# Kernel optimization log

Hardware: AMD Instinct MI355X
Metric: run time of the kernel (lower is better)

Reference implementation:

```python
import jax, jax.numpy as jnp
import numpy as np

N_NODES = 50000
HIDDEN = 64
N_EDGES = 1200000


def setup_inputs() -> dict:
    key = jax.random.key(0)
    ks = jax.random.split(key, 12)
    x = jax.random.normal(ks[0], (N_NODES, HIDDEN), dtype=jnp.float32)
    edge_index = jax.random.randint(ks[1], (2, N_EDGES), 0, N_NODES, dtype=jnp.int64)
    s = 1.0 / np.sqrt(HIDDEN)
    # RGCN layer (single relation): relation weight, root weight, bias
    W_rel1 = jax.random.normal(ks[2], (HIDDEN, HIDDEN), dtype=jnp.float32) * s
    W_root1 = jax.random.normal(ks[3], (HIDDEN, HIDDEN), dtype=jnp.float32) * s
    b1 = jnp.zeros((HIDDEN,), dtype=jnp.float32)
    # Three GraphConv layers: self weight, neighbor weight, bias each
    W_self2 = jax.random.normal(ks[4], (HIDDEN, HIDDEN), dtype=jnp.float32) * s
    W_nbr2 = jax.random.normal(ks[5], (HIDDEN, HIDDEN), dtype=jnp.float32) * s
    b2 = jnp.zeros((HIDDEN,), dtype=jnp.float32)
    W_self3 = jax.random.normal(ks[6], (HIDDEN, HIDDEN), dtype=jnp.float32) * s
    W_nbr3 = jax.random.normal(ks[7], (HIDDEN, HIDDEN), dtype=jnp.float32) * s
    b3 = jnp.zeros((HIDDEN,), dtype=jnp.float32)
    W_self4 = jax.random.normal(ks[8], (HIDDEN, HIDDEN), dtype=jnp.float32) * s
    W_nbr4 = jax.random.normal(ks[9], (HIDDEN, HIDDEN), dtype=jnp.float32) * s
    b4 = jnp.zeros((HIDDEN,), dtype=jnp.float32)
    return {
        "x": x, "edge_index": edge_index,
        "W_rel1": W_rel1, "W_root1": W_root1, "b1": b1,
        "W_self2": W_self2, "W_nbr2": W_nbr2, "b2": b2,
        "W_self3": W_self3, "W_nbr3": W_nbr3, "b3": b3,
        "W_self4": W_self4, "W_nbr4": W_nbr4, "b4": b4,
    }


def _rgcn(x, W_rel, W_root, b, src, dst, n_nodes):
    # single-relation RGCN: root transform + mean-aggregated relation transform
    msg = x[src] @ W_rel                                   # [E, H]
    agg = jax.ops.segment_sum(msg, dst, num_segments=n_nodes)
    cnt = jax.ops.segment_sum(jnp.ones((src.shape[0],), x.dtype), dst, num_segments=n_nodes)
    agg = agg / jnp.maximum(cnt, 1.0)[:, None]
    return x @ W_root + agg + b


def _graphconv(x, W_self, W_nbr, b, src, dst, n_nodes):
    # GraphConv: self transform + sum-aggregated neighbor transform
    agg = jax.ops.segment_sum(x[src], dst, num_segments=n_nodes)  # [N, H]
    return x @ W_self + agg @ W_nbr + b


def reference(x, edge_index, W_rel1, W_root1, b1, W_self2, W_nbr2, b2,
              W_self3, W_nbr3, b3, W_self4, W_nbr4, b4):
    n = x.shape[0]
    src, dst = edge_index[0], edge_index[1]
    h = jax.nn.relu(_rgcn(x, W_rel1, W_root1, b1, src, dst, n))
    h = jax.nn.relu(_graphconv(h, W_self2, W_nbr2, b2, src, dst, n))
    x_1 = h
    h = jax.nn.relu(_graphconv(h, W_self3, W_nbr3, b3, src, dst, n))
    h = jax.nn.relu(_graphconv(h, W_self4, W_nbr4, b4, src, dst, n))
    x_2 = h
    return (x_1, x_2)
```

## Files before the change

kernel.cpp:

```cpp
#include <hip/hip_runtime.h>
#include <hip/hip_fp16.h>

#define N_NODES 50000
#define HIDDEN  64
#define N_EDGES 1200000

#define BSHIFT 7
#define BUKSZ  128
#define NBUK   391
#define GBIN   256
#define PAD2   6144
#define FWAVES 12500
#define FBLK   (FWAVES / 4)
#define NPW    4

typedef unsigned short ushort_t;
typedef _Float16 hf2 __attribute__((ext_vector_type(2)));

__device__ __forceinline__ float bcastf(float v, int k) {
    return __int_as_float(__builtin_amdgcn_readlane(__float_as_int(v), k));
}
__device__ __forceinline__ hf2 u2h(unsigned u) { union { unsigned u; hf2 h; } x; x.u = u; return x.h; }
__device__ __forceinline__ unsigned h2u(hf2 h) { union { hf2 h; unsigned u; } x; x.h = h; return x.u; }
__device__ __forceinline__ unsigned pkh(float a, float b) {
    __half2 h = __float22half2_rn(make_float2(a, b));
    union { __half2 h; unsigned u; } x; x.h = h; return x.u;
}
__device__ __forceinline__ ushort_t f2h(float a) {
    __half h = __float2half_rn(a);
    union { __half h; ushort_t u; } x; x.h = h; return x.u;
}
__device__ __forceinline__ void bfly(float4& a) {
    a.x += __shfl_xor(a.x, 16); a.y += __shfl_xor(a.y, 16);
    a.z += __shfl_xor(a.z, 16); a.w += __shfl_xor(a.w, 16);
    a.x += __shfl_xor(a.x, 32); a.y += __shfl_xor(a.y, 32);
    a.z += __shfl_xor(a.z, 32); a.w += __shfl_xor(a.w, 32);
}

__global__ __launch_bounds__(512) void init_kernel(int* __restrict__ cursor,
                                                   const float* __restrict__ Wn2, const float* __restrict__ Ws2,
                                                   const float* __restrict__ Wn3, const float* __restrict__ Ws3,
                                                   const float* __restrict__ Wn4, const float* __restrict__ Ws4,
                                                   uint4* __restrict__ pw) {
    int b = blockIdx.x, tid = threadIdx.x;
    if (b == 0) {
        if (tid < NBUK) cursor[tid] = tid * PAD2;
    } else {
        int layer = b - 1;
        const float* Wn = (layer == 0) ? Wn2 : (layer == 1) ? Wn3 : Wn4;
        const float* Ws = (layer == 0) ? Ws2 : (layer == 1) ? Ws3 : Ws4;
        int kp = tid >> 4, q = tid & 15;
        {
            const float4 a = *(const float4*)(Wn + (2 * kp) * 64 + 4 * q);
            const float4 c = *(const float4*)(Wn + (2 * kp + 1) * 64 + 4 * q);
            pw[layer * 1024 + tid] = make_uint4(pkh(a.x, c.x), pkh(a.y, c.y), pkh(a.z, c.z), pkh(a.w, c.w));
        }
        {
            const float4 a = *(const float4*)(Ws + (2 * kp) * 64 + 4 * q);
            const float4 c = *(const float4*)(Ws + (2 * kp + 1) * 64 + 4 * q);
            pw[layer * 1024 + 512 + tid] = make_uint4(pkh(a.x, c.x), pkh(a.y, c.y), pkh(a.z, c.z), pkh(a.w, c.w));
        }
    }
}

__global__ __launch_bounds__(256) void scatter_fused_kernel(const int* __restrict__ ei,
                                                            int* __restrict__ cursor,
                                                            int* __restrict__ tmp, int E) {
    __shared__ int h[NBUK];
    __shared__ int cur[NBUK];
    int tid = threadIdx.x;
    for (int b = tid; b < NBUK; b += 256) h[b] = 0;
    __syncthreads();
    for (int e = blockIdx.x * 256 + tid; e < E; e += GBIN * 256)
        atomicAdd(&h[ei[E + e] >> BSHIFT], 1);
    __syncthreads();
    for (int b = tid; b < NBUK; b += 256) cur[b] = atomicAdd(&cursor[b], h[b]);
    __syncthreads();
    for (int e = blockIdx.x * 256 + tid; e < E; e += GBIN * 256) {
        int src = ei[e];
        int dst = ei[E + e];
        int p = atomicAdd(&cur[dst >> BSHIFT], 1);
        tmp[p] = src | ((dst & (BUKSZ - 1)) << 16);
    }
}

__global__ __launch_bounds__(512) void bucketize_kernel(const int* __restrict__ tmp,
                                                        const int* __restrict__ cursor,
                                                        int2* __restrict__ row_info,
                                                        ushort_t* __restrict__ csr,
                                                        const float* __restrict__ x,
                                                        const float* __restrict__ Wrel,
                                                        const float* __restrict__ Wroot,
                                                        const float* __restrict__ bias,
                                                        ushort_t* __restrict__ tbf,
                                                        ushort_t* __restrict__ ubf) {
    __shared__ int hist[BUKSZ];
    __shared__ int cur[BUKSZ];
    __shared__ ushort_t stage[PAD2];
    int b = blockIdx.x, tid = threadIdx.x;
    if (b < NBUK) {
        int base = b * PAD2;
        int count = cursor[b] - base;
        int node_base = b << BSHIFT;
        if (tid < BUKSZ) hist[tid] = 0;
        __syncthreads();
        for (int i = tid; i < count; i += 512)
            atomicAdd(&hist[tmp[base + i] >> 16], 1);
        __syncthreads();
        int v = (tid < BUKSZ) ? hist[tid] : 0;
        int vr = (v + 15) & ~15;
        __syncthreads();
        if (tid < BUKSZ) hist[tid] = vr;
#pragma unroll
        for (int o = 1; o < BUKSZ; o <<= 1) {
            __syncthreads();
            int y = (tid >= o && tid < BUKSZ) ? hist[tid - o] : 0;
            __syncthreads();
            if (tid < BUKSZ) hist[tid] += y;
        }
        __syncthreads();
        int excl = 0;
        if (tid < BUKSZ) {
            excl = hist[tid] - vr;
            cur[tid] = excl;
            int node = node_base + tid;
            if (node < N_NODES) row_info[node] = make_int2(base + excl, v);
        }
        __syncthreads();
        if (tid < BUKSZ) {
            for (int p = v; p < vr; ++p) stage[excl + p] = (ushort_t)N_NODES;
        }
        for (int i = tid; i < count; i += 512) {
            int p = tmp[base + i];
            int slot = atomicAdd(&cur[p >> 16], 1);
            stage[slot] = (ushort_t)(p & 0xFFFF);
        }
        __syncthreads();
        int total = hist[BUKSZ - 1];
        for (int i = tid; i < total; i += 512)
            csr[base + i] = stage[i];
    } else {
        int lane = tid & 63;
        float wn[64], ws[64];
#pragma unroll
        for (int k = 0; k < 64; ++k) {
            wn[k] = Wrel[k * 64 + lane];
            ws[k] = Wroot[k * 64 + lane];
        }
        float bv = bias[lane];
        int wave = (b - NBUK) * 8 + (tid >> 6);
        int nwaves = (gridDim.x - NBUK) * 8;
        if (wave == 0) tbf[(size_t)N_NODES * 64 + lane] = 0;
        for (int i = wave; i < N_NODES; i += nwaves) {
            float hv = x[i * 64 + lane];
            float tacc = 0.f, uacc = bv;
#pragma unroll
            for (int k = 0; k < 64; ++k) {
                float hk = bcastf(hv, k);
                tacc = fmaf(hk, wn[k], tacc);
                uacc = fmaf(hk, ws[k], uacc);
            }
            tbf[(size_t)i * 64 + lane] = f2h(tacc);
            ubf[(size_t)i * 64 + lane] = f2h(uacc);
        }
    }
}

__device__ __forceinline__ float4 agg_core(const ushort_t* __restrict__ tbf,
                                           const ushort_t* __restrict__ csr,
                                           int start, int deg, int g, int q) {
    const ushort_t* cp = csr + start;
    hf2 l0{0,0}, l1{0,0}, l2{0,0}, l3{0,0};
    hf2 m0{0,0}, m1{0,0}, m2{0,0}, m3{0,0};
    int vr = (deg + 15) & ~15;
    for (int base = 0; base < vr; base += 16) {
        int m = base + 4 * g;
        const uint2 iv = *(const uint2*)(cp + m);
        int s0 = (int)(iv.x & 0xFFFF);
        int s1 = (int)(iv.x >> 16);
        int s2 = (int)(iv.y & 0xFFFF);
        int s3 = (int)(iv.y >> 16);
        const uint2 w0 = *(const uint2*)(tbf + (size_t)s0 * 64 + q * 4);
        const uint2 w1 = *(const uint2*)(tbf + (size_t)s1 * 64 + q * 4);
        const uint2 w2 = *(const uint2*)(tbf + (size_t)s2 * 64 + q * 4);
        const uint2 w3 = *(const uint2*)(tbf + (size_t)s3 * 64 + q * 4);
        l0 += u2h(w0.x); m0 += u2h(w0.y);
        l1 += u2h(w1.x); m1 += u2h(w1.y);
        l2 += u2h(w2.x); m2 += u2h(w2.y);
        l3 += u2h(w3.x); m3 += u2h(w3.y);
    }
    hf2 lo = (l0 + l1) + (l2 + l3);
    hf2 hi = (m0 + m1) + (m2 + m3);
    float4 acc = make_float4((float)lo.x, (float)lo.y, (float)hi.x, (float)hi.y);
    bfly(acc);
    return acc;
}

__device__ __forceinline__ float4 unpack_u(const ushort_t* __restrict__ ubf, int node, int q) {
    const uint2 uv = *(const uint2*)(ubf + (size_t)node * 64 + q * 4);
    hf2 a = u2h(uv.x), b = u2h(uv.y);
    return make_float4((float)a.x, (float)a.y, (float)b.x, (float)b.y);
}

__global__ __launch_bounds__(256, 6) void fused_kernel(const ushort_t* __restrict__ tin,
                                                       const ushort_t* __restrict__ uin,
                                                       const int2* __restrict__ row_info,
                                                       const ushort_t* __restrict__ csr,
                                                       const uint4* __restrict__ pwL,
                                                       const float* __restrict__ bias_next,
                                                       ushort_t* __restrict__ tout,
                                                       ushort_t* __restrict__ uout,
                                                       float* __restrict__ dout,
                                                       int use_mean) {
    __shared__ uint4 wlds[1024];
    __shared__ float blds[64];
    int tid = threadIdx.x;
    for (int i = tid; i < 1024; i += 256) wlds[i] = pwL[i];
    if (tid < 64) blds[tid] = bias_next[tid];
    if (blockIdx.x == 0 && tid < 32)
        ((unsigned*)(tout + (size_t)N_NODES * 64))[tid] = 0;
    __syncthreads();
    int lane = tid & 63, g = lane >> 4, q = lane & 15;
    int w = blockIdx.x * 4 + (tid >> 6);

#pragma unroll
    for (int i = 0; i < NPW; ++i) {
        int node = w + FWAVES * i;
        if (node >= N_NODES) continue;
        int2 ri = row_info[node];
        float4 acc = agg_core(tin, csr, ri.x, ri.y, g, q);
        float sc = use_mean ? 1.f / fmaxf((float)ri.y, 1.f) : 1.f;
        const float4 uv = unpack_u(uin, node, q);
        float4 h;
        h.x = fmaxf(uv.x + acc.x * sc, 0.f);
        h.y = fmaxf(uv.y + acc.y * sc, 0.f);
        h.z = fmaxf(uv.z + acc.z * sc, 0.f);
        h.w = fmaxf(uv.w + acc.w * sc, 0.f);
        if (dout && g == 0)
            *(float4*)(dout + (size_t)node * 64 + q * 4) = h;
        int hp_lo = (int)pkh(h.x, h.y);
        int hp_hi = (int)pkh(h.z, h.w);
        float4 tp{0,0,0,0}, up{0,0,0,0};
#pragma unroll
        for (int jp = 0; jp < 8; ++jp) {
            int kp = 8 * g + jp;
            const uint4 wvn = wlds[kp * 16 + q];
            const uint4 wvs = wlds[512 + kp * 16 + q];
            int srcl = 4 * g + (jp >> 1);
            unsigned hu = (unsigned)__shfl((jp & 1) ? hp_hi : hp_lo, srcl);
            hf2 hh = u2h(hu);
            tp.x = __builtin_amdgcn_fdot2(hh, u2h(wvn.x), tp.x, false);
            tp.y = __builtin_amdgcn_fdot2(hh, u2h(wvn.y), tp.y, false);
            tp.z = __builtin_amdgcn_fdot2(hh, u2h(wvn.z), tp.z, false);
            tp.w = __builtin_amdgcn_fdot2(hh, u2h(wvn.w), tp.w, false);
            up.x = __builtin_amdgcn_fdot2(hh, u2h(wvs.x), up.x, false);
            up.y = __builtin_amdgcn_fdot2(hh, u2h(wvs.y), up.y, false);
            up.z = __builtin_amdgcn_fdot2(hh, u2h(wvs.z), up.z, false);
            up.w = __builtin_amdgcn_fdot2(hh, u2h(wvs.w), up.w, false);
        }
        bfly(tp); bfly(up);
        if (g == 0) {
            const float4 bv = *(const float4*)&blds[q * 4];
            uint2 upk, tpk;
            upk.x = pkh(up.x + bv.x, up.y + bv.y);
            upk.y = pkh(up.z + bv.z, up.w + bv.w);
            tpk.x = pkh(tp.x, tp.y);
            tpk.y = pkh(tp.z, tp.w);
            *(uint2*)(uout + (size_t)node * 64 + q * 4) = upk;
            *(uint2*)(tout + (size_t)node * 64 + q * 4) = tpk;
        }
    }
}

__global__ __launch_bounds__(256, 8) void agg_kernel(const ushort_t* __restrict__ tbf,
                                                     const ushort_t* __restrict__ ubf,
                                                     const int2* __restrict__ row_info,
                                                     const ushort_t* __restrict__ csr,
                                                     float* __restrict__ out, int use_mean) {
    int lane = threadIdx.x & 63;
    int g = lane >> 4, q = lane & 15;
    int node = (blockIdx.x * 256 + threadIdx.x) >> 6;
    if (node >= N_NODES) return;
    int2 ri = row_info[node];
    float4 acc = agg_core(tbf, csr, ri.x, ri.y, g, q);
    float scale = use_mean ? 1.f / fmaxf((float)ri.y, 1.f) : 1.f;
    if (g == 0) {
        const float4 uv = unpack_u(ubf, node, q);
        float4 r;
        r.x = fmaxf(uv.x + acc.x * scale, 0.f);
        r.y = fmaxf(uv.y + acc.y * scale, 0.f);
        r.z = fmaxf(uv.z + acc.z * scale, 0.f);
        r.w = fmaxf(uv.w + acc.w * scale, 0.f);
        *(float4*)(out + (size_t)node * 64 + q * 4) = r;
    }
}

extern "C" void kernel_launch(void* const* d_in, const int* in_sizes, int n_in,
                              void* d_out, int out_size, void* d_ws, size_t ws_size,
                              hipStream_t stream) {
    const float* x      = (const float*)d_in[0];
    const int*   ei     = (const int*)d_in[1];
    const float* Wrel1  = (const float*)d_in[2];
    const float* Wroot1 = (const float*)d_in[3];
    const float* b1     = (const float*)d_in[4];
    const float* Wself2 = (const float*)d_in[5];
    const float* Wnbr2  = (const float*)d_in[6];
    const float* b2     = (const float*)d_in[7];
    const float* Wself3 = (const float*)d_in[8];
    const float* Wnbr3  = (const float*)d_in[9];
    const float* b3     = (const float*)d_in[10];
    const float* Wself4 = (const float*)d_in[11];
    const float* Wnbr4  = (const float*)d_in[12];
    const float* b4     = (const float*)d_in[13];

    const int N = N_NODES, E = N_EDGES;

    auto align = [](size_t o) { return (o + 255) & ~(size_t)255; };
    char* base = (char*)d_ws;
    size_t off = 0;
    int*  cursor   = (int*)(base + off);  off = align(off + (size_t)NBUK * 4);
    int2* row_info = (int2*)(base + off); off = align(off + (size_t)N * 8);
    int*  tmp      = (int*)(base + off);  off = align(off + (size_t)NBUK * PAD2 * 4);
    ushort_t* csr  = (ushort_t*)(base + off); off = align(off + (size_t)NBUK * PAD2 * 2 + 1024);
    uint4* pw      = (uint4*)(base + off);    off = align(off + (size_t)3 * 1024 * 16);
    ushort_t* tbA  = (ushort_t*)(base + off); off = align(off + (size_t)(N + 1) * 64 * 2);
    ushort_t* tbB  = (ushort_t*)(base + off); off = align(off + (size_t)(N + 1) * 64 * 2);
    ushort_t* ubA  = (ushort_t*)(base + off); off = align(off + (size_t)N * 64 * 2);
    ushort_t* ubB  = (ushort_t*)(base + off); off = align(off + (size_t)N * 64 * 2);

    float* out1 = (float*)d_out;
    float* out2 = (float*)d_out + (size_t)N * 64;

    init_kernel<<<4, 512, 0, stream>>>(cursor, Wnbr2, Wself2, Wnbr3, Wself3, Wnbr4, Wself4, pw);
    scatter_fused_kernel<<<GBIN, 256, 0, stream>>>(ei, cursor, tmp, E);
    bucketize_kernel<<<NBUK + 1024, 512, 0, stream>>>(tmp, cursor, row_info, csr,
                                                      x, Wrel1, Wroot1, b1, tbA, ubA);
    fused_kernel<<<FBLK, 256, 0, stream>>>(tbA, ubA, row_info, csr, pw,        b2, tbB, ubB, nullptr, 1);
    fused_kernel<<<FBLK, 256, 0, stream>>>(tbB, ubB, row_info, csr, pw + 1024, b3, tbA, ubA, out1, 0);
    fused_kernel<<<FBLK, 256, 0, stream>>>(tbA, ubA, row_info, csr, pw + 2048, b4, tbB, ubB, nullptr, 0);
    agg_kernel<<<(N + 3) / 4, 256, 0, stream>>>(tbB, ubB, row_info, csr, out2, 0);
}
```

Measured before the change: 280.0 us.

## Map four nodes per wave, one per 16-lane group, with prefetched gather

Aggregation now gives each 16-lane group its own node, so one wave processes four nodes at once. It no longer splits one node's edges across groups and combines them with a cross-lane butterfly reduction. The gather loop is software-pipelined: the next four neighbour rows are prefetched while the current ones are summed, and out-of-range slots point at a zero pad row. The per-wave loop bound is the maximum padded degree across the four groups, which can leave some groups idle on skewed degrees. Per-node accumulation now goes into fp32 after each batch of four, the dense transform loops over the four nodes via shuffles, and the scatter grid width is doubled.

```diff
diff --git a/kernel.cpp b/kernel.cpp
--- a/kernel.cpp
+++ b/kernel.cpp
@@ -8,11 +8,10 @@
 #define BSHIFT 7
 #define BUKSZ  128
 #define NBUK   391
-#define GBIN   256
+#define GBIN   512
 #define PAD2   6144
 #define FWAVES 12500
 #define FBLK   (FWAVES / 4)
-#define NPW    4
 
 typedef unsigned short ushort_t;
 typedef _Float16 hf2 __attribute__((ext_vector_type(2)));
@@ -166,34 +165,44 @@
     }
 }
 
-__device__ __forceinline__ float4 agg_core(const ushort_t* __restrict__ tbf,
-                                           const ushort_t* __restrict__ csr,
-                                           int start, int deg, int g, int q) {
-    const ushort_t* cp = csr + start;
-    hf2 l0{0,0}, l1{0,0}, l2{0,0}, l3{0,0};
-    hf2 m0{0,0}, m1{0,0}, m2{0,0}, m3{0,0};
-    int vr = (deg + 15) & ~15;
-    for (int base = 0; base < vr; base += 16) {
-        int m = base + 4 * g;
-        const uint2 iv = *(const uint2*)(cp + m);
-        int s0 = (int)(iv.x & 0xFFFF);
-        int s1 = (int)(iv.x >> 16);
-        int s2 = (int)(iv.y & 0xFFFF);
-        int s3 = (int)(iv.y >> 16);
-        const uint2 w0 = *(const uint2*)(tbf + (size_t)s0 * 64 + q * 4);
-        const uint2 w1 = *(const uint2*)(tbf + (size_t)s1 * 64 + q * 4);
-        const uint2 w2 = *(const uint2*)(tbf + (size_t)s2 * 64 + q * 4);
-        const uint2 w3 = *(const uint2*)(tbf + (size_t)s3 * 64 + q * 4);
-        l0 += u2h(w0.x); m0 += u2h(w0.y);
-        l1 += u2h(w1.x); m1 += u2h(w1.y);
-        l2 += u2h(w2.x); m2 += u2h(w2.y);
-        l3 += u2h(w3.x); m3 += u2h(w3.y);
-    }
-    hf2 lo = (l0 + l1) + (l2 + l3);
-    hf2 hi = (m0 + m1) + (m2 + m3);
-    float4 acc = make_float4((float)lo.x, (float)lo.y, (float)hi.x, (float)hi.y);
-    bfly(acc);
-    return acc;
+__device__ __forceinline__ uint2 ldrow(const ushort_t* __restrict__ tbf, int s, int q) {
+    return *(const uint2*)(tbf + (size_t)s * 64 + q * 4);
+}
+
+__device__ __forceinline__ float4 agg_group(const ushort_t* __restrict__ tbf,
+                                            const ushort_t* __restrict__ csr,
+                                            int start, int vr, int vm, int q) {
+    float ax = 0.f, ay = 0.f, az = 0.f, aw = 0.f;
+    if (vm > 0) {
+        const ushort_t* cp = csr + start;
+        int inb = (0 < vr);
+        uint2 iv = *(const uint2*)cp;
+        int s0 = inb ? (int)(iv.x & 0xFFFF) : N_NODES;
+        int s1 = inb ? (int)(iv.x >> 16)    : N_NODES;
+        int s2 = inb ? (int)(iv.y & 0xFFFF) : N_NODES;
+        int s3 = inb ? (int)(iv.y >> 16)    : N_NODES;
+        uint2 c0 = ldrow(tbf, s0, q), c1 = ldrow(tbf, s1, q);
+        uint2 c2 = ldrow(tbf, s2, q), c3 = ldrow(tbf, s3, q);
+        uint2 ivn = *(const uint2*)(cp + ((4 < vr) ? 4 : 0));
+        for (int base = 4; base < vm; base += 4) {
+            int inb2 = (base < vr);
+            int t0 = inb2 ? (int)(ivn.x & 0xFFFF) : N_NODES;
+            int t1 = inb2 ? (int)(ivn.x >> 16)    : N_NODES;
+            int t2 = inb2 ? (int)(ivn.y & 0xFFFF) : N_NODES;
+            int t3 = inb2 ? (int)(ivn.y >> 16)    : N_NODES;
+            uint2 n0 = ldrow(tbf, t0, q), n1 = ldrow(tbf, t1, q);
+            uint2 n2 = ldrow(tbf, t2, q), n3 = ldrow(tbf, t3, q);
+            uint2 iv2 = *(const uint2*)(cp + ((base + 4 < vr) ? base + 4 : 0));
+            hf2 lo = (u2h(c0.x) + u2h(c1.x)) + (u2h(c2.x) + u2h(c3.x));
+            hf2 hi = (u2h(c0.y) + u2h(c1.y)) + (u2h(c2.y) + u2h(c3.y));
+            ax += (float)lo.x; ay += (float)lo.y; az += (float)hi.x; aw += (float)hi.y;
+            c0 = n0; c1 = n1; c2 = n2; c3 = n3; ivn = iv2;
+        }
+        hf2 lo = (u2h(c0.x) + u2h(c1.x)) + (u2h(c2.x) + u2h(c3.x));
+        hf2 hi = (u2h(c0.y) + u2h(c1.y)) + (u2h(c2.y) + u2h(c3.y));
+        ax += (float)lo.x; ay += (float)lo.y; az += (float)hi.x; aw += (float)hi.y;
+    }
+    return make_float4(ax, ay, az, aw);
 }
 
 __device__ __forceinline__ float4 unpack_u(const ushort_t* __restrict__ ubf, int node, int q) {
@@ -222,31 +231,35 @@
     __syncthreads();
     int lane = tid & 63, g = lane >> 4, q = lane & 15;
     int w = blockIdx.x * 4 + (tid >> 6);
-
-#pragma unroll
-    for (int i = 0; i < NPW; ++i) {
-        int node = w + FWAVES * i;
-        if (node >= N_NODES) continue;
-        int2 ri = row_info[node];
-        float4 acc = agg_core(tin, csr, ri.x, ri.y, g, q);
-        float sc = use_mean ? 1.f / fmaxf((float)ri.y, 1.f) : 1.f;
-        const float4 uv = unpack_u(uin, node, q);
-        float4 h;
-        h.x = fmaxf(uv.x + acc.x * sc, 0.f);
-        h.y = fmaxf(uv.y + acc.y * sc, 0.f);
-        h.z = fmaxf(uv.z + acc.z * sc, 0.f);
-        h.w = fmaxf(uv.w + acc.w * sc, 0.f);
-        if (dout && g == 0)
-            *(float4*)(dout + (size_t)node * 64 + q * 4) = h;
-        int hp_lo = (int)pkh(h.x, h.y);
-        int hp_hi = (int)pkh(h.z, h.w);
-        float4 tp{0,0,0,0}, up{0,0,0,0};
+    int node = 4 * w + g;
+
+    int2 ri = row_info[node];
+    int vr = (ri.y + 15) & ~15;
+    int o  = __shfl_xor(vr, 16); int vm = (o > vr) ? o : vr;
+    o = __shfl_xor(vm, 32); vm = (o > vm) ? o : vm;
+
+    float4 acc = agg_group(tin, csr, ri.x, vr, vm, q);
+    float sc = use_mean ? 1.f / fmaxf((float)ri.y, 1.f) : 1.f;
+    const float4 uv = unpack_u(uin, node, q);
+    float4 h;
+    h.x = fmaxf(uv.x + acc.x * sc, 0.f);
+    h.y = fmaxf(uv.y + acc.y * sc, 0.f);
+    h.z = fmaxf(uv.z + acc.z * sc, 0.f);
+    h.w = fmaxf(uv.w + acc.w * sc, 0.f);
+    if (dout)
+        *(float4*)(dout + (size_t)node * 64 + q * 4) = h;
+    int hp_lo = (int)pkh(h.x, h.y);
+    int hp_hi = (int)pkh(h.z, h.w);
+
+    uint2 tpk = make_uint2(0, 0), upk = make_uint2(0, 0);
+    for (int n = 0; n < 4; ++n) {
+        float4 tp{0, 0, 0, 0}, up{0, 0, 0, 0};
 #pragma unroll
         for (int jp = 0; jp < 8; ++jp) {
             int kp = 8 * g + jp;
             const uint4 wvn = wlds[kp * 16 + q];
             const uint4 wvs = wlds[512 + kp * 16 + q];
-            int srcl = 4 * g + (jp >> 1);
+            int srcl = 16 * n + 4 * g + (jp >> 1);
             unsigned hu = (unsigned)__shfl((jp & 1) ? hp_hi : hp_lo, srcl);
             hf2 hh = u2h(hu);
             tp.x = __builtin_amdgcn_fdot2(hh, u2h(wvn.x), tp.x, false);
@@ -259,17 +272,16 @@
             up.w = __builtin_amdgcn_fdot2(hh, u2h(wvs.w), up.w, false);
         }
         bfly(tp); bfly(up);
-        if (g == 0) {
+        if (g == n) {
             const float4 bv = *(const float4*)&blds[q * 4];
-            uint2 upk, tpk;
             upk.x = pkh(up.x + bv.x, up.y + bv.y);
             upk.y = pkh(up.z + bv.z, up.w + bv.w);
             tpk.x = pkh(tp.x, tp.y);
             tpk.y = pkh(tp.z, tp.w);
-            *(uint2*)(uout + (size_t)node * 64 + q * 4) = upk;
-            *(uint2*)(tout + (size_t)node * 64 + q * 4) = tpk;
-        }
-    }
+        }
+    }
+    *(uint2*)(uout + (size_t)node * 64 + q * 4) = upk;
+    *(uint2*)(tout + (size_t)node * 64 + q * 4) = tpk;
 }
 
 __global__ __launch_bounds__(256, 8) void agg_kernel(const ushort_t* __restrict__ tbf,
@@ -277,22 +289,23 @@
                                                      const int2* __restrict__ row_info,
                                                      const ushort_t* __restrict__ csr,
                                                      float* __restrict__ out, int use_mean) {
-    int lane = threadIdx.x & 63;
-    int g = lane >> 4, q = lane & 15;
-    int node = (blockIdx.x * 256 + threadIdx.x) >> 6;
-    if (node >= N_NODES) return;
+    int tid = threadIdx.x;
+    int lane = tid & 63, g = lane >> 4, q = lane & 15;
+    int wv = blockIdx.x * 4 + (tid >> 6);
+    int node = 4 * wv + g;
     int2 ri = row_info[node];
-    float4 acc = agg_core(tbf, csr, ri.x, ri.y, g, q);
+    int vr = (ri.y + 15) & ~15;
+    int o  = __shfl_xor(vr, 16); int vm = (o > vr) ? o : vr;
+    o = __shfl_xor(vm, 32); vm = (o > vm) ? o : vm;
+    float4 acc = agg_group(tbf, csr, ri.x, vr, vm, q);
     float scale = use_mean ? 1.f / fmaxf((float)ri.y, 1.f) : 1.f;
-    if (g == 0) {
-        const float4 uv = unpack_u(ubf, node, q);
-        float4 r;
-        r.x = fmaxf(uv.x + acc.x * scale, 0.f);
-        r.y = fmaxf(uv.y + acc.y * scale, 0.f);
-        r.z = fmaxf(uv.z + acc.z * scale, 0.f);
-        r.w = fmaxf(uv.w + acc.w * scale, 0.f);
-        *(float4*)(out + (size_t)node * 64 + q * 4) = r;
-    }
+    const float4 uv = unpack_u(ubf, node, q);
+    float4 r;
+    r.x = fmaxf(uv.x + acc.x * scale, 0.f);
+    r.y = fmaxf(uv.y + acc.y * scale, 0.f);
+    r.z = fmaxf(uv.z + acc.z * scale, 0.f);
+    r.w = fmaxf(uv.w + acc.w * scale, 0.f);
+    *(float4*)(out + (size_t)node * 64 + q * 4) = r;
 }
 
 extern "C" void kernel_launch(void* const* d_in, const int* in_sizes, int n_in,
@@ -338,5 +351,5 @@
     fused_kernel<<<FBLK, 256, 0, stream>>>(tbA, ubA, row_info, csr, pw,        b2, tbB, ubB, nullptr, 1);
     fused_kernel<<<FBLK, 256, 0, stream>>>(tbB, ubB, row_info, csr, pw + 1024, b3, tbA, ubA, out1, 0);
     fused_kernel<<<FBLK, 256, 0, stream>>>(tbA, ubA, row_info, csr, pw + 2048, b4, tbB, ubB, nullptr, 0);
-    agg_kernel<<<(N + 3) / 4, 256, 0, stream>>>(tbB, ubB, row_info, csr, out2, 0);
-}
+    agg_kernel<<<FBLK, 256, 0, stream>>>(tbB, ubB, row_info, csr, out2, 0);
+}
```

After: 340.4 us. 1.22x slower.
